# Optimization experiments

Hardware: AMD Instinct MI355X
Metric: run time of the kernel (lower is better)

Reference implementation:

```python
import jax, jax.numpy as jnp
import numpy as np

DIM = 256          # dim_m == dim_d (required by hist @ W1)
HIST = 200         # history_num
B = 2048
U_TOT = 100000
V_TOT = 100000
EPS = 1e-12


def _max_norm_lookup(table, idx):
    # torch nn.Embedding(max_norm=1): rows are renormalized to L2 norm <= 1 at lookup.
    g = table[idx]
    n = jnp.linalg.norm(g, axis=-1, keepdims=True)
    return g * jnp.minimum(1.0, 1.0 / jnp.maximum(n, EPS))


def _l2norm(x):
    # F.normalize(x, 2, -1)
    return x / jnp.maximum(jnp.linalg.norm(x, axis=-1, keepdims=True), EPS)


def setup_inputs() -> dict:
    key = jax.random.key(0)
    ks = jax.random.split(key, 12)
    xav = float(np.sqrt(6.0 / (DIM + DIM)))
    xav_pb = float(np.sqrt(6.0 / (HIST + DIM)))
    return {
        "batch_u": jax.random.randint(ks[0], (B,), 0, U_TOT),
        "batch_v": jax.random.randint(ks[1], (B,), 0, V_TOT),
        "batch_history": jax.random.randint(ks[2], (B, HIST), 0, V_TOT),
        "batch_olc": jax.random.randint(ks[3], (B,), 0, 68),
        "batch_cluster_olc": jax.random.randint(ks[4], (B,), 0, 68),
        "user_emb": jax.random.normal(ks[5], (U_TOT, DIM), jnp.float32),
        "venue_emb": jax.random.normal(ks[6], (V_TOT, DIM), jnp.float32),
        "W1": jax.random.uniform(ks[7], (DIM, DIM), jnp.float32, -xav, xav),
        "W2": jax.random.uniform(ks[8], (DIM, DIM), jnp.float32, -xav, xav),
        "P": jax.random.normal(ks[9], (HIST, DIM), jnp.float32),
        "bias": jax.random.uniform(ks[10], (HIST, DIM), jnp.float32, -xav_pb, xav_pb),
        "a": jax.random.normal(ks[11], (1,), jnp.float32),
    }


def reference(batch_u, batch_v, batch_history, batch_olc, batch_cluster_olc,
              user_emb, venue_emb, W1, W2, P, bias, a):
    # batch_olc / batch_cluster_olc are read but unused in the original forward.
    u = _max_norm_lookup(user_emb, batch_u)            # [B, D]
    v = _max_norm_lookup(venue_emb, batch_v)           # [B, D]
    hist = _max_norm_lookup(venue_emb, batch_history)  # [B, H, D]

    # h = tanh(hist @ W1 + (P @ W2) + bias), broadcast over batch
    h = jnp.tanh(jnp.einsum('bhd,de->bhe', hist, W1) + (P @ W2)[None] + bias[None])
    alpha = jax.nn.softmax(h, axis=1)                  # softmax over history dim
    l = jnp.sum(alpha * hist, axis=1) + a              # [B, D], scalar a broadcast

    # TransE-style score with p_norm = 2
    s = _l2norm(u) + _l2norm(l) - _l2norm(v)
    return jnp.sqrt(jnp.sum(s * s, axis=-1))           # [B]
```

## Files before the change

### kernel.cpp

```cpp
#include <hip/hip_runtime.h>
#include <hip/hip_bf16.h>

#define DIM 256
#define HIST 200
#define MPAD2 224
#define CHROWS 112
#define BATCH 2048
#define HSTRIDE 280
#define EPSF 1e-12f

typedef __bf16 bf16x8 __attribute__((ext_vector_type(8)));
typedef float f32x4 __attribute__((ext_vector_type(4)));

__device__ __forceinline__ unsigned short f2bf(float f) {
    union { float f; unsigned u; } v; v.f = f;
    unsigned r = (v.u + 0x7fffu + ((v.u >> 16) & 1u)) >> 16;
    return (unsigned short)r;
}
__device__ __forceinline__ unsigned pkbf(float a, float b) {
    __hip_bfloat162 t = __float22bfloat162_rn(float2{a, b});
    union { __hip_bfloat162 h; unsigned u; } v; v.h = t; return v.u;
}
__device__ __forceinline__ float bf_lo(unsigned u) {
    union { unsigned u; float f; } v; v.u = u << 16; return v.f;
}
__device__ __forceinline__ float bf_hi(unsigned u) {
    union { unsigned u; float f; } v; v.u = u & 0xffff0000u; return v.f;
}

__global__ __launch_bounds__(256) void k_prep(
    const float* __restrict__ W1, const float* __restrict__ P,
    const float* __restrict__ W2, const float* __restrict__ bias,
    const float* __restrict__ venue,
    unsigned short* __restrict__ W1t2, float* __restrict__ Ct2,
    float* __restrict__ sInv, int nV) {
    const int bid = blockIdx.x, tid = threadIdx.x;
    if (bid < 16) {
#pragma unroll
        for (int it = 0; it < 16; ++it) {
            int idx = bid * 4096 + it * 256 + tid;
            int g = idx >> 11, rem = idx & 2047;
            int n = rem >> 3, j = rem & 7;
            W1t2[idx] = f2bf(W1[(g * 8 + j) * DIM + n]);
        }
    } else if (bid < 240) {
        const int h = bid - 16;
        __shared__ float Prow[DIM];
        const int e = tid;
        float acc = 0.f;
        if (h < HIST) {
            Prow[e] = P[h * DIM + e];
            __syncthreads();
            acc = bias[h * DIM + e];
#pragma unroll 8
            for (int d = 0; d < DIM; ++d) acc += Prow[d] * W2[d * DIM + e];
        }
        Ct2[((h >> 4) * 4 + ((h >> 2) & 3)) * 1024 + e * 4 + (h & 3)] = acc;
    } else {
        const int lane = tid & 63;
        for (int row = (bid - 240) * 4 + (tid >> 6); row < nV; row += 1024) {
            const float4 g = *(const float4*)(venue + (size_t)row * DIM + lane * 4);
            float ss = g.x * g.x + g.y * g.y + g.z * g.z + g.w * g.w;
#pragma unroll
            for (int off = 32; off > 0; off >>= 1) ss += __shfl_xor(ss, off);
            if (lane == 0) sInv[row] = fminf(1.f, 1.f / fmaxf(sqrtf(ss), EPSF));
        }
    }
}

__global__ __launch_bounds__(512, 4) void k_main(
    const int* __restrict__ batch_u, const int* __restrict__ batch_v,
    const int* __restrict__ batch_history,
    const float* __restrict__ user_emb, const float* __restrict__ venue_emb,
    const float* __restrict__ Ct2, const unsigned short* __restrict__ W1t2,
    const float* __restrict__ sInv,
    const float* __restrict__ a_ptr, float* __restrict__ out) {

    __shared__ unsigned short histS[CHROWS * HSTRIDE];
    __shared__ float scaleS[MPAD2];
    __shared__ int idxS[MPAD2];
    __shared__ float lArr[DIM];
    __shared__ float redS[4][4];
    __shared__ float invS[3];

    const int b = blockIdx.x;
    const int tid = threadIdx.x;
    const int wave = tid >> 6;
    const int lane = tid & 63;
    const int quad = lane >> 4;
    const int l16 = lane & 15;
    const int n0 = wave * 32 + l16 * 2;

    if (tid < MPAD2) {
        int m = (tid < HIST) ? tid : 0;
        int ix = batch_history[b * HIST + m];
        idxS[tid] = ix;
        scaleS[tid] = (tid < HIST) ? sInv[ix] : 0.f;
    }
    float ut = 0.f, vt = 0.f;
    if (tid < DIM) {
        ut = user_emb[(size_t)batch_u[b] * DIM + tid];
        vt = venue_emb[(size_t)batch_v[b] * DIM + tid];
    }
    __syncthreads();

    const float a_val = a_ptr[0];
    float Ssum[2] = {0.f, 0.f}, Lnum[2] = {0.f, 0.f};

    for (int chunk = 0; chunk < 2; ++chunk) {
        const int base = chunk * CHROWS;
        const int r0 = wave * 14;
#pragma unroll
        for (int half = 0; half < 2; ++half) {
            float4 buf[7];
#pragma unroll
            for (int j = 0; j < 7; ++j)
                buf[j] = *(const float4*)(venue_emb +
                         (size_t)idxS[base + r0 + half * 7 + j] * DIM + lane * 4);
#pragma unroll
            for (int j = 0; j < 7; ++j) {
                int lr = r0 + half * 7 + j;
                float s = scaleS[base + lr];
                uint2 pk = { pkbf(buf[j].x * s, buf[j].y * s),
                             pkbf(buf[j].z * s, buf[j].w * s) };
                *(uint2*)&histS[lr * HSTRIDE + lane * 4] = pk;
            }
        }
        f32x4 acc[7][2];
#pragma unroll
        for (int t = 0; t < 7; ++t)
#pragma unroll
            for (int i = 0; i < 2; ++i)
                acc[t][i] = *(const f32x4*)(Ct2 + ((chunk * 7 + t) * 4 + quad) * 1024 + (n0 + i) * 4);
        __syncthreads();

#pragma unroll
        for (int k = 0; k < 8; ++k) {
            bf16x8 Bf0 = *(const bf16x8*)(const void*)(W1t2 + (k * 4 + quad) * 2048 + n0 * 8);
            bf16x8 Bf1 = *(const bf16x8*)(const void*)(W1t2 + (k * 4 + quad) * 2048 + (n0 + 1) * 8);
#pragma unroll
            for (int t = 0; t < 7; ++t) {
                const bf16x8 Af =
                    *(const bf16x8*)(const void*)(&histS[(t * 16 + l16) * HSTRIDE + k * 32 + quad * 8]);
                acc[t][0] = __builtin_amdgcn_mfma_f32_16x16x32_bf16(Af, Bf0, acc[t][0], 0, 0, 0);
                acc[t][1] = __builtin_amdgcn_mfma_f32_16x16x32_bf16(Af, Bf1, acc[t][1], 0, 0, 0);
            }
        }

#pragma unroll
        for (int t = 0; t < 7; ++t)
#pragma unroll
            for (int r = 0; r < 4; ++r) {
                int lm = t * 16 + quad * 4 + r;
                if (base + lm < HIST) {
                    unsigned hv = *(const unsigned*)&histS[lm * HSTRIDE + n0];
                    float x0 = acc[t][0][r], x1 = acc[t][1][r];
                    float th0 = 1.f - 2.f * __builtin_amdgcn_rcpf(__expf(2.f * x0) + 1.f);
                    float th1 = 1.f - 2.f * __builtin_amdgcn_rcpf(__expf(2.f * x1) + 1.f);
                    float e0 = __expf(th0), e1 = __expf(th1);
                    Ssum[0] += e0; Lnum[0] += e0 * bf_lo(hv);
                    Ssum[1] += e1; Lnum[1] += e1 * bf_hi(hv);
                }
            }
        __syncthreads();
    }

#pragma unroll
    for (int i = 0; i < 2; ++i) {
        Ssum[i] += __shfl_xor(Ssum[i], 16); Ssum[i] += __shfl_xor(Ssum[i], 32);
        Lnum[i] += __shfl_xor(Lnum[i], 16); Lnum[i] += __shfl_xor(Lnum[i], 32);
    }
    if (quad == 0)
        *(float2*)&lArr[n0] = float2{ Lnum[0] * __builtin_amdgcn_rcpf(Ssum[0]) + a_val,
                                      Lnum[1] * __builtin_amdgcn_rcpf(Ssum[1]) + a_val };
    __syncthreads();

    const float lt = (tid < DIM) ? lArr[tid] : 0.f;
    float pu = ut * ut, pv = vt * vt, pl = lt * lt;
#pragma unroll
    for (int off = 32; off > 0; off >>= 1) {
        pu += __shfl_xor(pu, off);
        pv += __shfl_xor(pv, off);
        pl += __shfl_xor(pl, off);
    }
    if (lane == 0 && wave < 4) { redS[wave][0] = pu; redS[wave][1] = pv; redS[wave][2] = pl; }
    __syncthreads();
    if (tid == 0) {
        float su = 0.f, sv = 0.f, sl = 0.f;
        for (int w = 0; w < 4; ++w) { su += redS[w][0]; sv += redS[w][1]; sl += redS[w][2]; }
        invS[0] = 1.f / fmaxf(sqrtf(su), EPSF);
        invS[1] = 1.f / fmaxf(sqrtf(sv), EPSF);
        invS[2] = 1.f / fmaxf(sqrtf(sl), EPSF);
    }
    __syncthreads();
    float s = ut * invS[0] + lt * invS[2] - vt * invS[1];
    float s2 = s * s;
#pragma unroll
    for (int off = 32; off > 0; off >>= 1) s2 += __shfl_xor(s2, off);
    if (lane == 0 && wave < 4) redS[wave][3] = s2;
    __syncthreads();
    if (tid == 0) out[b] = sqrtf(redS[0][3] + redS[1][3] + redS[2][3] + redS[3][3]);
}

extern "C" void kernel_launch(void* const* d_in, const int* in_sizes, int n_in,
                              void* d_out, int out_size, void* d_ws, size_t ws_size,
                              hipStream_t stream) {
    const int* batch_u = (const int*)d_in[0];
    const int* batch_v = (const int*)d_in[1];
    const int* batch_history = (const int*)d_in[2];
    const float* user_emb = (const float*)d_in[5];
    const float* venue_emb = (const float*)d_in[6];
    const float* W1 = (const float*)d_in[7];
    const float* W2 = (const float*)d_in[8];
    const float* P = (const float*)d_in[9];
    const float* bias = (const float*)d_in[10];
    const float* a = (const float*)d_in[11];
    float* out = (float*)d_out;

    const int nV = in_sizes[6] / DIM;

    float* Ct2 = (float*)d_ws;
    unsigned short* W1t2 = (unsigned short*)((char*)d_ws + 229376);
    float* sInv = (float*)((char*)d_ws + 229376 + 131072);

    k_prep<<<496, 256, 0, stream>>>(W1, P, W2, bias, venue_emb, W1t2, Ct2, sInv, nV);
    k_main<<<BATCH, 512, 0, stream>>>(batch_u, batch_v, batch_history,
                                      user_emb, venue_emb, Ct2, W1t2, sInv, a, out);
}
```

Before: 480.3 us.

## Compute history row norms in-kernel, drop full-table norm pass, swizzle LDS

Drops the prep pass that computed max-norm scales for every row of the 100k-row venue table and instead computes each gathered history row's norm inside the main kernel with a wave shuffle reduction and rsq. The LDS history tile moves from a padded stride to an XOR-swizzled 256-wide layout to avoid bank conflicts, and the second chunk processes only 6 tiles (208 rows) instead of 7. Launch bounds drop from 4 to 2 blocks per SM hint. The cost is extra shuffles per gathered row and different register/occupancy behaviour.

```diff
diff --git a/kernel.cpp b/kernel.cpp
--- a/kernel.cpp
+++ b/kernel.cpp
@@ -3,10 +3,8 @@
 
 #define DIM 256
 #define HIST 200
-#define MPAD2 224
-#define CHROWS 112
+#define MROWS 208
 #define BATCH 2048
-#define HSTRIDE 280
 #define EPSF 1e-12f
 
 typedef __bf16 bf16x8 __attribute__((ext_vector_type(8)));
@@ -31,9 +29,7 @@
 __global__ __launch_bounds__(256) void k_prep(
     const float* __restrict__ W1, const float* __restrict__ P,
     const float* __restrict__ W2, const float* __restrict__ bias,
-    const float* __restrict__ venue,
-    unsigned short* __restrict__ W1t2, float* __restrict__ Ct2,
-    float* __restrict__ sInv, int nV) {
+    unsigned short* __restrict__ W1t2, float* __restrict__ Ct2) {
     const int bid = blockIdx.x, tid = threadIdx.x;
     if (bid < 16) {
 #pragma unroll
@@ -43,7 +39,7 @@
             int n = rem >> 3, j = rem & 7;
             W1t2[idx] = f2bf(W1[(g * 8 + j) * DIM + n]);
         }
-    } else if (bid < 240) {
+    } else {
         const int h = bid - 16;
         __shared__ float Prow[DIM];
         const int e = tid;
@@ -55,30 +51,94 @@
 #pragma unroll 8
             for (int d = 0; d < DIM; ++d) acc += Prow[d] * W2[d * DIM + e];
         }
-        Ct2[((h >> 4) * 4 + ((h >> 2) & 3)) * 1024 + e * 4 + (h & 3)] = acc;
-    } else {
-        const int lane = tid & 63;
-        for (int row = (bid - 240) * 4 + (tid >> 6); row < nV; row += 1024) {
-            const float4 g = *(const float4*)(venue + (size_t)row * DIM + lane * 4);
+        if (h < 224)
+            Ct2[((h >> 4) * 4 + ((h >> 2) & 3)) * 1024 + e * 4 + (h & 3)] = acc;
+    }
+}
+
+template<int TILES>
+__device__ __forceinline__ void process_chunk(
+    int chunk_base, const int* idxS, const float* __restrict__ venue_emb,
+    unsigned short* histS, const float* __restrict__ Ct2,
+    const unsigned short* __restrict__ W1t2,
+    int wave, int lane, int quad, int l16, int n0,
+    float a_val, float* Ssum, float* Lnum) {
+
+    const int HALF = TILES;
+    const int r0 = wave * 2 * TILES;
+#pragma unroll
+    for (int half = 0; half < 2; ++half) {
+        float4 buf[HALF];
+#pragma unroll
+        for (int j = 0; j < HALF; ++j)
+            buf[j] = *(const float4*)(venue_emb +
+                     (size_t)idxS[chunk_base + r0 + half * HALF + j] * DIM + lane * 4);
+#pragma unroll
+        for (int j = 0; j < HALF; ++j) {
+            int lr = r0 + half * HALF + j;
+            int m = chunk_base + lr;
+            float4 g = buf[j];
             float ss = g.x * g.x + g.y * g.y + g.z * g.z + g.w * g.w;
-#pragma unroll
-            for (int off = 32; off > 0; off >>= 1) ss += __shfl_xor(ss, off);
-            if (lane == 0) sInv[row] = fminf(1.f, 1.f / fmaxf(sqrtf(ss), EPSF));
-        }
-    }
-}
-
-__global__ __launch_bounds__(512, 4) void k_main(
+            ss += __shfl_xor(ss, 1);  ss += __shfl_xor(ss, 2);  ss += __shfl_xor(ss, 4);
+            ss += __shfl_xor(ss, 8);  ss += __shfl_xor(ss, 16); ss += __shfl_xor(ss, 32);
+            float s = (ss > 1.f) ? __builtin_amdgcn_rsqf(ss) : 1.f;
+            if (m >= HIST) s = 0.f;
+            uint2 pk = { pkbf(g.x * s, g.y * s), pkbf(g.z * s, g.w * s) };
+            int gr = (lane >> 1) ^ (lr & 7);
+            *(uint2*)&histS[lr * 256 + gr * 8 + (lane & 1) * 4] = pk;
+        }
+    }
+    __syncthreads();
+
+    f32x4 acc[TILES][2];
+#pragma unroll
+    for (int t = 0; t < TILES; ++t)
+#pragma unroll
+        for (int i = 0; i < 2; ++i)
+            acc[t][i] = *(const f32x4*)(Ct2 + (((chunk_base >> 4) + t) * 4 + quad) * 1024 + (n0 + i) * 4);
+
+#pragma unroll
+    for (int k = 0; k < 8; ++k) {
+        bf16x8 Bf0 = *(const bf16x8*)(const void*)(W1t2 + (k * 4 + quad) * 2048 + n0 * 8);
+        bf16x8 Bf1 = *(const bf16x8*)(const void*)(W1t2 + (k * 4 + quad) * 2048 + (n0 + 1) * 8);
+#pragma unroll
+        for (int t = 0; t < TILES; ++t) {
+            int gr = (k * 4 + quad) ^ (l16 & 7);
+            const bf16x8 Af = *(const bf16x8*)(const void*)(&histS[(t * 16 + l16) * 256 + gr * 8]);
+            acc[t][0] = __builtin_amdgcn_mfma_f32_16x16x32_bf16(Af, Bf0, acc[t][0], 0, 0, 0);
+            acc[t][1] = __builtin_amdgcn_mfma_f32_16x16x32_bf16(Af, Bf1, acc[t][1], 0, 0, 0);
+        }
+    }
+
+#pragma unroll
+    for (int t = 0; t < TILES; ++t)
+#pragma unroll
+        for (int r = 0; r < 4; ++r) {
+            int lm = t * 16 + quad * 4 + r;
+            int m = chunk_base + lm;
+            if (m < HIST) {
+                int gr = (wave * 4 + (l16 >> 2)) ^ (lm & 7);
+                unsigned hv = *(const unsigned*)&histS[lm * 256 + gr * 8 + (l16 & 3) * 2];
+                float x0 = acc[t][0][r], x1 = acc[t][1][r];
+                float th0 = 1.f - 2.f * __builtin_amdgcn_rcpf(__expf(2.f * x0) + 1.f);
+                float th1 = 1.f - 2.f * __builtin_amdgcn_rcpf(__expf(2.f * x1) + 1.f);
+                float e0 = __expf(th0), e1 = __expf(th1);
+                Ssum[0] += e0; Lnum[0] += e0 * bf_lo(hv);
+                Ssum[1] += e1; Lnum[1] += e1 * bf_hi(hv);
+            }
+        }
+    __syncthreads();
+}
+
+__global__ __launch_bounds__(512, 2) void k_main(
     const int* __restrict__ batch_u, const int* __restrict__ batch_v,
     const int* __restrict__ batch_history,
     const float* __restrict__ user_emb, const float* __restrict__ venue_emb,
     const float* __restrict__ Ct2, const unsigned short* __restrict__ W1t2,
-    const float* __restrict__ sInv,
     const float* __restrict__ a_ptr, float* __restrict__ out) {
 
-    __shared__ unsigned short histS[CHROWS * HSTRIDE];
-    __shared__ float scaleS[MPAD2];
-    __shared__ int idxS[MPAD2];
+    __shared__ __align__(16) unsigned short histS[112 * 256];
+    __shared__ int idxS[MROWS];
     __shared__ float lArr[DIM];
     __shared__ float redS[4][4];
     __shared__ float invS[3];
@@ -91,12 +151,8 @@
     const int l16 = lane & 15;
     const int n0 = wave * 32 + l16 * 2;
 
-    if (tid < MPAD2) {
-        int m = (tid < HIST) ? tid : 0;
-        int ix = batch_history[b * HIST + m];
-        idxS[tid] = ix;
-        scaleS[tid] = (tid < HIST) ? sInv[ix] : 0.f;
-    }
+    if (tid < MROWS)
+        idxS[tid] = batch_history[b * HIST + ((tid < HIST) ? tid : 0)];
     float ut = 0.f, vt = 0.f;
     if (tid < DIM) {
         ut = user_emb[(size_t)batch_u[b] * DIM + tid];
@@ -107,63 +163,10 @@
     const float a_val = a_ptr[0];
     float Ssum[2] = {0.f, 0.f}, Lnum[2] = {0.f, 0.f};
 
-    for (int chunk = 0; chunk < 2; ++chunk) {
-        const int base = chunk * CHROWS;
-        const int r0 = wave * 14;
-#pragma unroll
-        for (int half = 0; half < 2; ++half) {
-            float4 buf[7];
-#pragma unroll
-            for (int j = 0; j < 7; ++j)
-                buf[j] = *(const float4*)(venue_emb +
-                         (size_t)idxS[base + r0 + half * 7 + j] * DIM + lane * 4);
-#pragma unroll
-            for (int j = 0; j < 7; ++j) {
-                int lr = r0 + half * 7 + j;
-                float s = scaleS[base + lr];
-                uint2 pk = { pkbf(buf[j].x * s, buf[j].y * s),
-                             pkbf(buf[j].z * s, buf[j].w * s) };
-                *(uint2*)&histS[lr * HSTRIDE + lane * 4] = pk;
-            }
-        }
-        f32x4 acc[7][2];
-#pragma unroll
-        for (int t = 0; t < 7; ++t)
-#pragma unroll
-            for (int i = 0; i < 2; ++i)
-                acc[t][i] = *(const f32x4*)(Ct2 + ((chunk * 7 + t) * 4 + quad) * 1024 + (n0 + i) * 4);
-        __syncthreads();
-
-#pragma unroll
-        for (int k = 0; k < 8; ++k) {
-            bf16x8 Bf0 = *(const bf16x8*)(const void*)(W1t2 + (k * 4 + quad) * 2048 + n0 * 8);
-            bf16x8 Bf1 = *(const bf16x8*)(const void*)(W1t2 + (k * 4 + quad) * 2048 + (n0 + 1) * 8);
-#pragma unroll
-            for (int t = 0; t < 7; ++t) {
-                const bf16x8 Af =
-                    *(const bf16x8*)(const void*)(&histS[(t * 16 + l16) * HSTRIDE + k * 32 + quad * 8]);
-                acc[t][0] = __builtin_amdgcn_mfma_f32_16x16x32_bf16(Af, Bf0, acc[t][0], 0, 0, 0);
-                acc[t][1] = __builtin_amdgcn_mfma_f32_16x16x32_bf16(Af, Bf1, acc[t][1], 0, 0, 0);
-            }
-        }
-
-#pragma unroll
-        for (int t = 0; t < 7; ++t)
-#pragma unroll
-            for (int r = 0; r < 4; ++r) {
-                int lm = t * 16 + quad * 4 + r;
-                if (base + lm < HIST) {
-                    unsigned hv = *(const unsigned*)&histS[lm * HSTRIDE + n0];
-                    float x0 = acc[t][0][r], x1 = acc[t][1][r];
-                    float th0 = 1.f - 2.f * __builtin_amdgcn_rcpf(__expf(2.f * x0) + 1.f);
-                    float th1 = 1.f - 2.f * __builtin_amdgcn_rcpf(__expf(2.f * x1) + 1.f);
-                    float e0 = __expf(th0), e1 = __expf(th1);
-                    Ssum[0] += e0; Lnum[0] += e0 * bf_lo(hv);
-                    Ssum[1] += e1; Lnum[1] += e1 * bf_hi(hv);
-                }
-            }
-        __syncthreads();
-    }
+    process_chunk<7>(0,   idxS, venue_emb, histS, Ct2, W1t2,
+                     wave, lane, quad, l16, n0, a_val, Ssum, Lnum);
+    process_chunk<6>(112, idxS, venue_emb, histS, Ct2, W1t2,
+                     wave, lane, quad, l16, n0, a_val, Ssum, Lnum);
 
 #pragma unroll
     for (int i = 0; i < 2; ++i) {
@@ -217,13 +220,10 @@
     const float* a = (const float*)d_in[11];
     float* out = (float*)d_out;
 
-    const int nV = in_sizes[6] / DIM;
-
     float* Ct2 = (float*)d_ws;
     unsigned short* W1t2 = (unsigned short*)((char*)d_ws + 229376);
-    float* sInv = (float*)((char*)d_ws + 229376 + 131072);
-
-    k_prep<<<496, 256, 0, stream>>>(W1, P, W2, bias, venue_emb, W1t2, Ct2, sInv, nV);
+
+    k_prep<<<240, 256, 0, stream>>>(W1, P, W2, bias, W1t2, Ct2);
     k_main<<<BATCH, 512, 0, stream>>>(batch_u, batch_v, batch_history,
-                                      user_emb, venue_emb, Ct2, W1t2, sInv, a, out);
-}
+                                      user_emb, venue_emb, Ct2, W1t2, a, out);
+}
```

Result: faster. 420.5 us (-12.4%).
